# Kernel tuning notes

Hardware: AMD Instinct MI355X
Metric: run time of the kernel (lower is better)

Reference implementation:

```python
import jax, jax.numpy as jnp
import numpy as np

B, T, D, H = 2, 2048, 1024, 16
HS = D // H  # head_size = 64
EPS = 1e-5


def layer_norm(x, g, b):
    mu = jnp.mean(x, axis=-1, keepdims=True)
    var = jnp.var(x, axis=-1, keepdims=True)
    return (x - mu) * jax.lax.rsqrt(var + EPS) * g + b


def setup_inputs() -> dict:
    key = jax.random.key(0)
    ks = jax.random.split(key, 12)
    s_attn = 1.0 / np.sqrt(D)
    s_ff1 = 1.0 / np.sqrt(D)
    s_ff2 = 1.0 / np.sqrt(4 * D)
    return {
        "x": jax.random.normal(ks[0], (B, T, D), jnp.float32),
        "Wq": jax.random.normal(ks[1], (H, D, HS), jnp.float32) * s_attn,
        "Wk": jax.random.normal(ks[2], (H, D, HS), jnp.float32) * s_attn,
        "Wv": jax.random.normal(ks[3], (H, D, HS), jnp.float32) * s_attn,
        "Wo": jax.random.normal(ks[4], (H * HS, D), jnp.float32) * (1.0 / np.sqrt(H * HS)),
        "bo": jnp.zeros((D,), jnp.float32),
        "W1": jax.random.normal(ks[5], (D, 4 * D), jnp.float32) * s_ff1,
        "b1": jnp.zeros((4 * D,), jnp.float32),
        "W2": jax.random.normal(ks[6], (4 * D, D), jnp.float32) * s_ff2,
        "b2": jnp.zeros((D,), jnp.float32),
        "ln1_g": jnp.ones((D,), jnp.float32),
        "ln1_b": jnp.zeros((D,), jnp.float32),
        "ln2_g": jnp.ones((D,), jnp.float32),
        "ln2_b": jnp.zeros((D,), jnp.float32),
    }


def reference(x, Wq, Wk, Wv, Wo, bo, W1, b1, W2, b2, ln1_g, ln1_b, ln2_g, ln2_b):
    # --- self-attention on ln1(x) ---
    h = layer_norm(x, ln1_g, ln1_b)
    Q = jnp.einsum('bsd,hdk->bhsk', h, Wq)
    K = jnp.einsum('bsd,hdk->bhsk', h, Wk)
    V = jnp.einsum('bsd,hdk->bhsk', h, Wv)
    scores = jnp.einsum('bhqk,bhsk->bhqs', Q, K) * (HS ** -0.5)
    attn = jax.nn.softmax(scores, axis=-1)  # [B,H,T,T] non-causal, as in source
    out = jnp.einsum('bhqs,bhsk->bhqk', attn, V)
    out = out.transpose(0, 2, 1, 3).reshape(B, T, H * HS)  # concat heads
    sa = out @ Wo + bo
    x = x + sa
    # --- feed-forward on ln2(x) ---
    h2 = layer_norm(x, ln2_g, ln2_b)
    ff = jax.nn.relu(h2 @ W1 + b1) @ W2 + b2
    return x + ff
```

## Files before the change

kernel.cpp:

```cpp
#include <hip/hip_runtime.h>
#include <cstdint>
#include <cmath>

typedef __bf16 bf16;
typedef __bf16 bf16x8 __attribute__((ext_vector_type(8)));
typedef __bf16 bf16x4 __attribute__((ext_vector_type(4)));
typedef __bf16 bf16x2 __attribute__((ext_vector_type(2)));
typedef float  f32x4  __attribute__((ext_vector_type(4)));

#define B_   2
#define T_   2048
#define D_   1024
#define H_   16
#define HS_  64
#define NTOK (B_ * T_)

typedef __attribute__((address_space(1))) uint8_t* gp1_t;
typedef __attribute__((address_space(3))) uint8_t* lp3_t;
__device__ __forceinline__ void gl_lds16(const void* g, void* l) {
    __builtin_amdgcn_global_load_lds((gp1_t)(uintptr_t)g,
                                     (lp3_t)(uint32_t)(uintptr_t)l,
                                     16, 0, 0);
}

__device__ __forceinline__ f32x4 mfma16(bf16x8 a, bf16x8 b, f32x4 c) {
    return __builtin_amdgcn_mfma_f32_16x16x32_bf16(a, b, c, 0, 0, 0);
}

__device__ __forceinline__ uint32_t pk2(float lo, float hi) {
    bf16x2 t; t[0] = (bf16)lo; t[1] = (bf16)hi;
    return __builtin_bit_cast(uint32_t, t);
}
__device__ __forceinline__ void pl32(uint32_t& a, uint32_t& b) {
    asm("v_permlane32_swap_b32 %0, %1" : "+v"(a), "+v"(b));
}
__device__ __forceinline__ void pl16(uint32_t& a, uint32_t& b) {
    asm("v_permlane16_swap_b32 %0, %1" : "+v"(a), "+v"(b));
}

__global__ void tcast(const float* __restrict__ in, bf16* __restrict__ out,
                      int R, int C) {
    __shared__ float t[32][33];
    const int c0 = blockIdx.x * 32, r0 = blockIdx.y * 32;
    for (int i = 0; i < 4; i++) {
        int r = threadIdx.y + i * 8;
        t[r][threadIdx.x] = in[(size_t)(r0 + r) * C + c0 + threadIdx.x];
    }
    __syncthreads();
    for (int i = 0; i < 4; i++) {
        int rr = threadIdx.y + i * 8;
        out[(size_t)(c0 + rr) * R + r0 + threadIdx.x] = (bf16)t[threadIdx.x][rr];
    }
}

__global__ void qkv_pack(const float* __restrict__ Wq, const float* __restrict__ Wk,
                         const float* __restrict__ Wv, bf16* __restrict__ out) {
    const int z = blockIdx.z;
    const int qkv = z >> 4;
    const float* in = (qkv == 0 ? Wq : qkv == 1 ? Wk : Wv) + (size_t)(z & 15) * D_ * HS_;
    bf16* o = out + (size_t)z * HS_ * D_;
    __shared__ float t[32][33];
    const int c0 = blockIdx.x * 32, r0 = blockIdx.y * 32;
    for (int i = 0; i < 4; i++) {
        int r = threadIdx.y + i * 8;
        t[r][threadIdx.x] = in[(size_t)(r0 + r) * HS_ + c0 + threadIdx.x];
    }
    __syncthreads();
    for (int i = 0; i < 4; i++) {
        int rr = threadIdx.y + i * 8;
        o[(size_t)(c0 + rr) * D_ + r0 + threadIdx.x] = (bf16)t[threadIdx.x][rr];
    }
}

__global__ __launch_bounds__(256) void ln_kernel(const float* __restrict__ x,
                                                 const float* __restrict__ g,
                                                 const float* __restrict__ b,
                                                 bf16* __restrict__ out) {
    const int row = blockIdx.x;
    const int tid = threadIdx.x;
    const float4 v = ((const float4*)(x + (size_t)row * 1024))[tid];
    float s  = v.x + v.y + v.z + v.w;
    float s2 = v.x * v.x + v.y * v.y + v.z * v.z + v.w * v.w;
    for (int m = 1; m < 64; m <<= 1) {
        s  += __shfl_xor(s, m);
        s2 += __shfl_xor(s2, m);
    }
    __shared__ float rs[4], rq[4];
    const int lane = tid & 63, wv = tid >> 6;
    if (lane == 0) { rs[wv] = s; rq[wv] = s2; }
    __syncthreads();
    s  = rs[0] + rs[1] + rs[2] + rs[3];
    s2 = rq[0] + rq[1] + rq[2] + rq[3];
    const float mu   = s * (1.f / 1024.f);
    const float var  = s2 * (1.f / 1024.f) - mu * mu;
    const float rstd = rsqrtf(var + 1e-5f);
    const float4 gg = ((const float4*)g)[tid];
    const float4 bb = ((const float4*)b)[tid];
    bf16x4 o;
    o[0] = (bf16)((v.x - mu) * rstd * gg.x + bb.x);
    o[1] = (bf16)((v.y - mu) * rstd * gg.y + bb.y);
    o[2] = (bf16)((v.z - mu) * rstd * gg.z + bb.z);
    o[3] = (bf16)((v.w - mu) * rstd * gg.w + bb.w);
    *(bf16x4*)(out + (size_t)row * 1024 + tid * 4) = o;
}

__global__ __launch_bounds__(256) void combine4(const float* __restrict__ p0,
                                                const float* __restrict__ p1,
                                                const float* __restrict__ p2,
                                                const float* __restrict__ p3,
                                                const float* __restrict__ resid,
                                                const float* __restrict__ bias,
                                                float* __restrict__ out) {
    const int i4 = blockIdx.x * 256 + threadIdx.x;
    const float4 a = ((const float4*)p0)[i4];
    const float4 b = ((const float4*)p1)[i4];
    const float4 c = ((const float4*)p2)[i4];
    const float4 d = ((const float4*)p3)[i4];
    const float4 r = ((const float4*)resid)[i4];
    const float4 bb = ((const float4*)bias)[i4 & 255];
    float4 o;
    o.x = a.x + b.x + c.x + d.x + r.x + bb.x;
    o.y = a.y + b.y + c.y + d.y + r.y + bb.y;
    o.z = a.z + b.z + c.z + d.z + r.z + bb.z;
    o.w = a.w + b.w + c.w + d.w + r.w + bb.w;
    ((float4*)out)[i4] = o;
}

template <int BIAS, int RELU, int RES, int OUTBF16>
__global__ __launch_bounds__(256, 2) void gemm_bt(
    const bf16* __restrict__ A, const bf16* __restrict__ Bt,
    const float* __restrict__ bias, const float* __restrict__ resid,
    void* __restrict__ Cout, int M, int N, int K) {
    __shared__ __align__(16) bf16 As[2][128 * 32];
    __shared__ __align__(16) bf16 Bs[2][128 * 32];
    const int tid  = threadIdx.x;
    const int lane = tid & 63, w = tid >> 6;
    const int quad = lane >> 4, l15 = lane & 15;
    const int m0 = blockIdx.y * 128, n0 = blockIdx.x * 128;
    const int wm = (w & 1) * 64, wn = (w >> 1) * 64;

    f32x4 acc[4][4];
    for (int i = 0; i < 4; i++)
        for (int j = 0; j < 4; j++) acc[i][j] = f32x4{0.f, 0.f, 0.f, 0.f};

    const int arow = lane >> 2;
    const int acol = (lane & 3) * 8;
    const int c0 = w * 2, c1 = w * 2 + 1;

    for (int kt = 0; kt < K; kt += 64) {
        gl_lds16(A  + (size_t)(m0 + c0 * 16 + arow) * K + kt + acol,      &As[0][c0 * 512]);
        gl_lds16(A  + (size_t)(m0 + c1 * 16 + arow) * K + kt + acol,      &As[0][c1 * 512]);
        gl_lds16(A  + (size_t)(m0 + c0 * 16 + arow) * K + kt + 32 + acol, &As[1][c0 * 512]);
        gl_lds16(A  + (size_t)(m0 + c1 * 16 + arow) * K + kt + 32 + acol, &As[1][c1 * 512]);
        gl_lds16(Bt + (size_t)(n0 + c0 * 16 + arow) * K + kt + acol,      &Bs[0][c0 * 512]);
        gl_lds16(Bt + (size_t)(n0 + c1 * 16 + arow) * K + kt + acol,      &Bs[0][c1 * 512]);
        gl_lds16(Bt + (size_t)(n0 + c0 * 16 + arow) * K + kt + 32 + acol, &Bs[1][c0 * 512]);
        gl_lds16(Bt + (size_t)(n0 + c1 * 16 + arow) * K + kt + 32 + acol, &Bs[1][c1 * 512]);
        __syncthreads();
        for (int kh = 0; kh < 2; kh++) {
            bf16x8 af[4], bfr[4];
            for (int mi = 0; mi < 4; mi++)
                af[mi] = *(const bf16x8*)&As[kh][(wm + mi * 16 + l15) * 32 + quad * 8];
            for (int ni = 0; ni < 4; ni++)
                bfr[ni] = *(const bf16x8*)&Bs[kh][(wn + ni * 16 + l15) * 32 + quad * 8];
            for (int mi = 0; mi < 4; mi++)
                for (int ni = 0; ni < 4; ni++)
                    acc[mi][ni] = mfma16(af[mi], bfr[ni], acc[mi][ni]);
        }
        __syncthreads();
    }

    for (int mi = 0; mi < 4; mi++) {
        for (int ni = 0; ni < 4; ni++) {
            const int colb = n0 + wn + ni * 16 + l15;
            const float bv = BIAS ? bias[colb] : 0.f;
            for (int r = 0; r < 4; r++) {
                const int row = m0 + wm + mi * 16 + quad * 4 + r;
                float v = acc[mi][ni][r] + bv;
                if (RELU) v = fmaxf(v, 0.f);
                if (RES)  v += resid[(size_t)row * N + colb];
                if (OUTBF16) ((bf16*)Cout)[(size_t)row * N + colb] = (bf16)v;
                else         ((float*)Cout)[(size_t)row * N + colb] = v;
            }
        }
    }
}

template <int BIAS, int RELU, int VTP, int PARTIAL>
__global__ __launch_bounds__(512, 2) void gemm256(
    const bf16* __restrict__ A, const bf16* __restrict__ Bt,
    const float* __restrict__ bias, void* __restrict__ Cout,
    bf16* __restrict__ Vt, float* __restrict__ P0, float* __restrict__ P1,
    int M, int N, int K) {
    __shared__ __align__(16) bf16 Asub[4][256 * 32];
    __shared__ __align__(16) bf16 Bsub[4][256 * 32];
    const int tid  = threadIdx.x;
    const int lane = tid & 63, w = tid >> 6;
    const int wr = w >> 2, wc = w & 3;
    const int quad = lane >> 4, l15 = lane & 15;
    const int m0 = blockIdx.y * 256, n0 = blockIdx.x * 256;
    const int kpb = PARTIAL ? (K / (int)gridDim.z) : K;
    const int k0  = PARTIAL ? (int)blockIdx.z * kpb : 0;
    const int S   = kpb / 32;

    const int slog = (((lane & 3) ^ ((lane >> 3) & 3)) * 8);
    const int crow = lane >> 2;
    const bf16* gA0 = A  + (size_t)(m0 + 32 * w + crow)      * K + k0 + slog;
    const bf16* gA1 = A  + (size_t)(m0 + 32 * w + 16 + crow) * K + k0 + slog;
    const bf16* gB0 = Bt + (size_t)(n0 + 32 * w + crow)      * K + k0 + slog;
    const bf16* gB1 = Bt + (size_t)(n0 + 32 * w + 16 + crow) * K + k0 + slog;

    for (int t = 0; t < 3; t++) {
        gl_lds16(gA0, &Asub[t][(32 * w) * 32]);
        gl_lds16(gA1, &Asub[t][(32 * w + 16) * 32]);
        gl_lds16(gB0, &Bsub[t][(32 * w) * 32]);
        gl_lds16(gB1, &Bsub[t][(32 * w + 16) * 32]);
        gA0 += 32; gA1 += 32; gB0 += 32; gB1 += 32;
    }

    f32x4 acc[8][4];
#pragma unroll
    for (int i = 0; i < 8; i++)
#pragma unroll
        for (int j = 0; j < 4; j++) acc[i][j] = f32x4{0.f, 0.f, 0.f, 0.f};

    const int swz = (quad ^ ((l15 >> 1) & 3)) * 8;
    const int aof = (wr * 128 + l15) * 32 + swz;
    const int bof = (wc * 64 + l15) * 32 + swz;

    asm volatile("s_waitcnt vmcnt(8)" ::: "memory");
    __builtin_amdgcn_sched_barrier(0);
    __builtin_amdgcn_s_barrier();

    for (int s = 0; s < S; s++) {
        const bf16* Ab = &Asub[s & 3][0];
        const bf16* Bb = &Bsub[s & 3][0];
        const int pb = (s + 3) & 3;
        bf16x8 af[4], bfr[4];
#pragma unroll
        for (int f = 0; f < 4; f++) af[f] = *(const bf16x8*)&Ab[aof + f * 512];
#pragma unroll
        for (int n = 0; n < 4; n++) bfr[n] = *(const bf16x8*)&Bb[bof + n * 512];
        if (s + 3 < S) {
            gl_lds16(gA0, &Asub[pb][(32 * w) * 32]);
            gl_lds16(gA1, &Asub[pb][(32 * w + 16) * 32]);
            gA0 += 32; gA1 += 32;
        }
        __builtin_amdgcn_sched_barrier(0);
        __builtin_amdgcn_s_barrier();
        asm volatile("s_waitcnt lgkmcnt(0)" ::: "memory");
        __builtin_amdgcn_sched_barrier(0);
        __builtin_amdgcn_s_setprio(1);
#pragma unroll
        for (int f = 0; f < 4; f++)
#pragma unroll
            for (int n = 0; n < 4; n++)
                acc[f][n] = mfma16(af[f], bfr[n], acc[f][n]);
        __builtin_amdgcn_s_setprio(0);
        __builtin_amdgcn_sched_barrier(0);
        __builtin_amdgcn_s_barrier();
#pragma unroll
        for (int f = 0; f < 4; f++) af[f] = *(const bf16x8*)&Ab[aof + 2048 + f * 512];
        if (s + 3 < S) {
            gl_lds16(gB0, &Bsub[pb][(32 * w) * 32]);
            gl_lds16(gB1, &Bsub[pb][(32 * w + 16) * 32]);
            gB0 += 32; gB1 += 32;
        }
        __builtin_amdgcn_sched_barrier(0);
        __builtin_amdgcn_s_barrier();
        asm volatile("s_waitcnt lgkmcnt(0)" ::: "memory");
        __builtin_amdgcn_sched_barrier(0);
        __builtin_amdgcn_s_setprio(1);
#pragma unroll
        for (int f = 0; f < 4; f++)
#pragma unroll
            for (int n = 0; n < 4; n++)
                acc[4 + f][n] = mfma16(af[f], bfr[n], acc[4 + f][n]);
        __builtin_amdgcn_s_setprio(0);
        __builtin_amdgcn_sched_barrier(0);
        if (s <= S - 4)      asm volatile("s_waitcnt vmcnt(8)" ::: "memory");
        else if (s == S - 3) asm volatile("s_waitcnt vmcnt(4)" ::: "memory");
        else if (s == S - 2) asm volatile("s_waitcnt vmcnt(0)" ::: "memory");
        __builtin_amdgcn_s_barrier();
    }

#pragma unroll
    for (int mi = 0; mi < 8; mi++) {
#pragma unroll
        for (int ni = 0; ni < 4; ni++) {
            const int colb = n0 + wc * 64 + ni * 16 + l15;
            const int row0 = m0 + wr * 128 + (mi >> 2) * 64 + (mi & 3) * 16 + quad * 4;
            if (VTP && colb >= 2048) {
                const int h = (colb - 2048) >> 6, hs = (colb - 2048) & 63;
                const int b = row0 >> 11;
                bf16x4 p4;
                p4[0] = (bf16)acc[mi][ni][0];
                p4[1] = (bf16)acc[mi][ni][1];
                p4[2] = (bf16)acc[mi][ni][2];
                p4[3] = (bf16)acc[mi][ni][3];
                *(bf16x4*)&Vt[((size_t)(b * 16 + h) * 64 + hs) * T_ + (row0 & 2047)] = p4;
                continue;
            }
            if (PARTIAL) {
                float* Cz = ((int)blockIdx.z < 2 ? P0 : P1) + (size_t)(blockIdx.z & 1) * M * N;
                for (int r = 0; r < 4; r++)
                    Cz[(size_t)(row0 + r) * N + colb] = acc[mi][ni][r];
            } else {
                const float bv = BIAS ? bias[colb] : 0.f;
                for (int r = 0; r < 4; r++) {
                    float v = acc[mi][ni][r] + bv;
                    if (RELU) v = fmaxf(v, 0.f);
                    ((bf16*)Cout)[(size_t)(row0 + r) * N + colb] = (bf16)v;
                }
            }
        }
    }
}

#define LSTR 68
#define NJ   (T_ / 64)
__global__ __launch_bounds__(256, 2) void flash_attn(const bf16* __restrict__ QKV,
                                                     const bf16* __restrict__ Vt,
                                                     bf16* __restrict__ attn_out) {
    const int bh = blockIdx.y, b = bh >> 4, h = bh & 15;
    const int q0 = blockIdx.x * 128;
    const int tid = threadIdx.x, lane = tid & 63, w = tid >> 6;
    const int quad = lane >> 4, l15 = lane & 15;
    __shared__ __align__(16) bf16 Ks[2][64 * LSTR];
    __shared__ __align__(16) bf16 Vs[2][64 * LSTR];
    const bf16* Qb = QKV + (size_t)b * T_ * 3072 + h * 64;
    const bf16* Kb = QKV + (size_t)b * T_ * 3072 + 1024 + h * 64;
    const bf16* Vb = Vt  + (size_t)bh * HS_ * T_;

    const float sc = 0.125f * 1.44269504088896f;
    const int sr = tid >> 2, scc = (tid & 3) * 16;

    bf16x8 QA[2][2];
    for (int qnt = 0; qnt < 2; qnt++) {
        const size_t row = (size_t)(q0 + w * 32 + qnt * 16 + l15) * 3072;
        for (int kk = 0; kk < 2; kk++) {
            bf16x8 q = *(const bf16x8*)&Qb[row + kk * 32 + quad * 8];
            for (int i = 0; i < 8; i++) q[i] = (bf16)((float)q[i] * sc);
            QA[qnt][kk] = q;
        }
    }

    bf16x8 ones8;
    for (int i = 0; i < 8; i++) ones8[i] = (bf16)1.0f;

    f32x4 O[2][4], lacc[2];
    for (int mi = 0; mi < 2; mi++) {
        lacc[mi] = f32x4{0.f, 0.f, 0.f, 0.f};
        for (int n = 0; n < 4; n++) O[mi][n] = f32x4{0.f, 0.f, 0.f, 0.f};
    }

    *(bf16x8*)&Ks[0][sr * LSTR + scc]     = *(const bf16x8*)&Kb[(size_t)sr * 3072 + scc];
    *(bf16x8*)&Ks[0][sr * LSTR + scc + 8] = *(const bf16x8*)&Kb[(size_t)sr * 3072 + scc + 8];
    *(bf16x8*)&Vs[0][sr * LSTR + scc]     = *(const bf16x8*)&Vb[(size_t)sr * T_ + scc];
    *(bf16x8*)&Vs[0][sr * LSTR + scc + 8] = *(const bf16x8*)&Vb[(size_t)sr * T_ + scc + 8];
    __syncthreads();

    bf16x8 k0, k1, v0, v1;
    for (int j = 0; j < NJ; j++) {
        const int buf = j & 1;
        if (j + 1 < NJ) {
            const int s1 = (j + 1) * 64;
            k0 = *(const bf16x8*)&Kb[(size_t)(s1 + sr) * 3072 + scc];
            k1 = *(const bf16x8*)&Kb[(size_t)(s1 + sr) * 3072 + scc + 8];
            v0 = *(const bf16x8*)&Vb[(size_t)sr * T_ + s1 + scc];
            v1 = *(const bf16x8*)&Vb[(size_t)sr * T_ + s1 + scc + 8];
        }
        bf16x8 KB[4][2];
#pragma unroll
        for (int smt = 0; smt < 4; smt++)
#pragma unroll
            for (int kk = 0; kk < 2; kk++)
                KB[smt][kk] = *(const bf16x8*)&Ks[buf][(smt * 16 + l15) * LSTR + kk * 32 + quad * 8];

        bf16x8 PA[2][2];
#pragma unroll
        for (int qnt = 0; qnt < 2; qnt++) {
            f32x4 ST[4];
#pragma unroll
            for (int smt = 0; smt < 4; smt++) ST[smt] = f32x4{0.f, 0.f, 0.f, 0.f};
            __builtin_amdgcn_s_setprio(1);
#pragma unroll
            for (int kk = 0; kk < 2; kk++)
#pragma unroll
                for (int smt = 0; smt < 4; smt++)
                    ST[smt] = mfma16(KB[smt][kk], QA[qnt][kk], ST[smt]);
            __builtin_amdgcn_s_setprio(0);
            uint32_t w00 = pk2(__builtin_amdgcn_exp2f(ST[0][0]), __builtin_amdgcn_exp2f(ST[0][1]));
            uint32_t w01 = pk2(__builtin_amdgcn_exp2f(ST[0][2]), __builtin_amdgcn_exp2f(ST[0][3]));
            uint32_t w10 = pk2(__builtin_amdgcn_exp2f(ST[1][0]), __builtin_amdgcn_exp2f(ST[1][1]));
            uint32_t w11 = pk2(__builtin_amdgcn_exp2f(ST[1][2]), __builtin_amdgcn_exp2f(ST[1][3]));
            uint32_t w20 = pk2(__builtin_amdgcn_exp2f(ST[2][0]), __builtin_amdgcn_exp2f(ST[2][1]));
            uint32_t w21 = pk2(__builtin_amdgcn_exp2f(ST[2][2]), __builtin_amdgcn_exp2f(ST[2][3]));
            uint32_t w30 = pk2(__builtin_amdgcn_exp2f(ST[3][0]), __builtin_amdgcn_exp2f(ST[3][1]));
            uint32_t w31 = pk2(__builtin_amdgcn_exp2f(ST[3][2]), __builtin_amdgcn_exp2f(ST[3][3]));
            pl32(w00, w10); pl16(w00, w10);
            pl32(w01, w11); pl16(w01, w11);
            pl32(w20, w30); pl16(w20, w30);
            pl32(w21, w31); pl16(w21, w31);
            union { uint32_t u[4]; bf16x8 v; } pa0, pa1;
            pa0.u[0] = w00; pa0.u[1] = w01; pa0.u[2] = w10; pa0.u[3] = w11;
            pa1.u[0] = w20; pa1.u[1] = w21; pa1.u[2] = w30; pa1.u[3] = w31;
            PA[qnt][0] = pa0.v;
            PA[qnt][1] = pa1.v;
        }
        bf16x8 VB[4][2];
#pragma unroll
        for (int n = 0; n < 4; n++)
#pragma unroll
            for (int kk = 0; kk < 2; kk++)
                VB[n][kk] = *(const bf16x8*)&Vs[buf][(n * 16 + l15) * LSTR + kk * 32 + quad * 8];
        __builtin_amdgcn_s_setprio(1);
#pragma unroll
        for (int mi = 0; mi < 2; mi++) {
            const bf16x8 PA0 = PA[mi][0];
            const bf16x8 PA1 = PA[mi][1];
#pragma unroll
            for (int n = 0; n < 4; n++) {
                O[mi][n] = mfma16(PA0, VB[n][0], O[mi][n]);
                O[mi][n] = mfma16(PA1, VB[n][1], O[mi][n]);
            }
            lacc[mi] = mfma16(PA0, ones8, lacc[mi]);
            lacc[mi] = mfma16(PA1, ones8, lacc[mi]);
        }
        __builtin_amdgcn_s_setprio(0);
        if (j + 1 < NJ) {
            *(bf16x8*)&Ks[buf ^ 1][sr * LSTR + scc]     = k0;
            *(bf16x8*)&Ks[buf ^ 1][sr * LSTR + scc + 8] = k1;
            *(bf16x8*)&Vs[buf ^ 1][sr * LSTR + scc]     = v0;
            *(bf16x8*)&Vs[buf ^ 1][sr * LSTR + scc + 8] = v1;
        }
        __syncthreads();
    }

    for (int mi = 0; mi < 2; mi++) {
        for (int r = 0; r < 4; r++) {
            const float inv = 1.f / lacc[mi][r];
            const size_t tok = (size_t)b * T_ + q0 + w * 32 + mi * 16 + quad * 4 + r;
            for (int n = 0; n < 4; n++)
                attn_out[tok * 1024 + h * 64 + n * 16 + l15] = (bf16)(O[mi][n][r] * inv);
        }
    }
}

extern "C" void kernel_launch(void* const* d_in, const int* in_sizes, int n_in,
                              void* d_out, int out_size, void* d_ws, size_t ws_size,
                              hipStream_t stream) {
    const float* x   = (const float*)d_in[0];
    const float* Wq  = (const float*)d_in[1];
    const float* Wk  = (const float*)d_in[2];
    const float* Wv  = (const float*)d_in[3];
    const float* Wo  = (const float*)d_in[4];
    const float* bo  = (const float*)d_in[5];
    const float* W1  = (const float*)d_in[6];
    const float* b1  = (const float*)d_in[7];
    const float* W2  = (const float*)d_in[8];
    const float* b2  = (const float*)d_in[9];
    const float* g1  = (const float*)d_in[10];
    const float* be1 = (const float*)d_in[11];
    const float* g2  = (const float*)d_in[12];
    const float* be2 = (const float*)d_in[13];

    char* ws = (char*)d_ws;
    const size_t MB = 1ull << 20;
    bf16*  WqkvT = (bf16*)(ws);
    bf16*  WoT   = (bf16*)(ws + 6  * MB);
    bf16*  W1T   = (bf16*)(ws + 8  * MB);
    bf16*  W2T   = (bf16*)(ws + 16 * MB);
    bf16*  hbuf  = (bf16*)(ws + 24 * MB);
    bf16*  QKV   = (bf16*)(ws + 32 * MB);
    bf16*  Vt    = (bf16*)(ws + 56 * MB);
    bf16*  attn  = (bf16*)(ws + 64 * MB);
    float* x2    = (float*)(ws + 72 * MB);
    bf16*  ff1   = (bf16*)(ws + 32 * MB);
    float* partA = (float*)(ws);
    float* partB = (float*)(ws + 88 * MB);
    float* out   = (float*)d_out;

    dim3 tb(32, 8);
    qkv_pack<<<dim3(2, 32, 48), tb, 0, stream>>>(Wq, Wk, Wv, WqkvT);
    tcast<<<dim3(32, 32),  tb, 0, stream>>>(Wo, WoT, 1024, 1024);
    tcast<<<dim3(128, 32), tb, 0, stream>>>(W1, W1T, 1024, 4096);
    tcast<<<dim3(32, 128), tb, 0, stream>>>(W2, W2T, 4096, 1024);
    ln_kernel<<<NTOK, 256, 0, stream>>>(x, g1, be1, hbuf);
    gemm256<0, 0, 1, 0><<<dim3(12, 16), 512, 0, stream>>>(
        hbuf, WqkvT, nullptr, QKV, Vt, nullptr, nullptr, NTOK, 3072, 1024);
    flash_attn<<<dim3(T_ / 128, B_ * H_), 256, 0, stream>>>(QKV, Vt, attn);
    gemm_bt<1, 0, 1, 0><<<dim3(8, 32), 256, 0, stream>>>(attn, WoT, bo, x, x2, NTOK, 1024, 1024);
    ln_kernel<<<NTOK, 256, 0, stream>>>(x2, g2, be2, hbuf);
    gemm256<1, 1, 0, 0><<<dim3(16, 16), 512, 0, stream>>>(
        hbuf, W1T, b1, ff1, nullptr, nullptr, nullptr, NTOK, 4096, 1024);
    gemm256<0, 0, 0, 1><<<dim3(4, 16, 4), 512, 0, stream>>>(
        ff1, W2T, nullptr, nullptr, nullptr, partA, partB, NTOK, 1024, 4096);
    combine4<<<NTOK, 256, 0, stream>>>(partA, partA + (size_t)NTOK * 1024,
                                       partB, partB + (size_t)NTOK * 1024,
                                       x2, b2, out);
}
```

Measured before the change: 341.1 us.

## Fuse weight prep and LN1 into one launch; use 128-tile GEMM for QKV

Merges the four weight transpose/cast kernels and the first layernorm into a single launch, with branches selected by block index. This removes several launch gaps. The QKV projection moves from the 256-tile gemm256 kernel (192 blocks) to the 128-tile gemm_bt kernel (768 blocks), which gains a V-transpose epilogue so the machine's CUs are better filled. The trade-off is a smaller tile with less data reuse per block, and a divergent, heterogeneous prep kernel.

```diff
diff --git a/kernel.cpp b/kernel.cpp
--- a/kernel.cpp
+++ b/kernel.cpp
@@ -38,37 +38,79 @@
     asm("v_permlane16_swap_b32 %0, %1" : "+v"(a), "+v"(b));
 }
 
-__global__ void tcast(const float* __restrict__ in, bf16* __restrict__ out,
-                      int R, int C) {
+__global__ __launch_bounds__(256) void prep_fused(
+    const float* __restrict__ Wq, const float* __restrict__ Wk,
+    const float* __restrict__ Wv, const float* __restrict__ Wo,
+    const float* __restrict__ W1, const float* __restrict__ W2,
+    const float* __restrict__ x,  const float* __restrict__ g,
+    const float* __restrict__ be,
+    bf16* __restrict__ WqkvT, bf16* __restrict__ WoT,
+    bf16* __restrict__ W1T,  bf16* __restrict__ W2T,
+    bf16* __restrict__ hbuf) {
+    const int bid = blockIdx.x;
+    const int tid = threadIdx.x;
+
+    if (bid >= 12288) {
+        const int row = bid - 12288;
+        const float4 v = ((const float4*)(x + (size_t)row * 1024))[tid];
+        float s  = v.x + v.y + v.z + v.w;
+        float s2 = v.x * v.x + v.y * v.y + v.z * v.z + v.w * v.w;
+        for (int m = 1; m < 64; m <<= 1) {
+            s  += __shfl_xor(s, m);
+            s2 += __shfl_xor(s2, m);
+        }
+        __shared__ float rs[4], rq[4];
+        const int lane = tid & 63, wv = tid >> 6;
+        if (lane == 0) { rs[wv] = s; rq[wv] = s2; }
+        __syncthreads();
+        s  = rs[0] + rs[1] + rs[2] + rs[3];
+        s2 = rq[0] + rq[1] + rq[2] + rq[3];
+        const float mu   = s * (1.f / 1024.f);
+        const float var  = s2 * (1.f / 1024.f) - mu * mu;
+        const float rstd = rsqrtf(var + 1e-5f);
+        const float4 gg = ((const float4*)g)[tid];
+        const float4 bb = ((const float4*)be)[tid];
+        bf16x4 o;
+        o[0] = (bf16)((v.x - mu) * rstd * gg.x + bb.x);
+        o[1] = (bf16)((v.y - mu) * rstd * gg.y + bb.y);
+        o[2] = (bf16)((v.z - mu) * rstd * gg.z + bb.z);
+        o[3] = (bf16)((v.w - mu) * rstd * gg.w + bb.w);
+        *(bf16x4*)(hbuf + (size_t)row * 1024 + tid * 4) = o;
+        return;
+    }
+
+    const float* in; bf16* out;
+    int C, R, bx, by;
+    if (bid < 3072) {
+        const int z = bid >> 6, rem = bid & 63;
+        bx = rem & 1; by = rem >> 1;
+        C = HS_; R = D_;
+        in  = (z < 16 ? Wq : z < 32 ? Wk : Wv) + (size_t)(z & 15) * D_ * HS_;
+        out = WqkvT + (size_t)z * HS_ * D_;
+    } else if (bid < 4096) {
+        const int rem = bid - 3072;
+        bx = rem & 31; by = rem >> 5;
+        C = 1024; R = 1024; in = Wo; out = WoT;
+    } else if (bid < 8192) {
+        const int rem = bid - 4096;
+        bx = rem & 127; by = rem >> 7;
+        C = 4096; R = 1024; in = W1; out = W1T;
+    } else {
+        const int rem = bid - 8192;
+        bx = rem & 31; by = rem >> 5;
+        C = 1024; R = 4096; in = W2; out = W2T;
+    }
+    const int tx = tid & 31, ty = tid >> 5;
+    const int c0 = bx * 32, r0 = by * 32;
     __shared__ float t[32][33];
-    const int c0 = blockIdx.x * 32, r0 = blockIdx.y * 32;
     for (int i = 0; i < 4; i++) {
-        int r = threadIdx.y + i * 8;
-        t[r][threadIdx.x] = in[(size_t)(r0 + r) * C + c0 + threadIdx.x];
+        int r = ty + i * 8;
+        t[r][tx] = in[(size_t)(r0 + r) * C + c0 + tx];
     }
     __syncthreads();
     for (int i = 0; i < 4; i++) {
-        int rr = threadIdx.y + i * 8;
-        out[(size_t)(c0 + rr) * R + r0 + threadIdx.x] = (bf16)t[threadIdx.x][rr];
-    }
-}
-
-__global__ void qkv_pack(const float* __restrict__ Wq, const float* __restrict__ Wk,
-                         const float* __restrict__ Wv, bf16* __restrict__ out) {
-    const int z = blockIdx.z;
-    const int qkv = z >> 4;
-    const float* in = (qkv == 0 ? Wq : qkv == 1 ? Wk : Wv) + (size_t)(z & 15) * D_ * HS_;
-    bf16* o = out + (size_t)z * HS_ * D_;
-    __shared__ float t[32][33];
-    const int c0 = blockIdx.x * 32, r0 = blockIdx.y * 32;
-    for (int i = 0; i < 4; i++) {
-        int r = threadIdx.y + i * 8;
-        t[r][threadIdx.x] = in[(size_t)(r0 + r) * HS_ + c0 + threadIdx.x];
-    }
-    __syncthreads();
-    for (int i = 0; i < 4; i++) {
-        int rr = threadIdx.y + i * 8;
-        o[(size_t)(c0 + rr) * D_ + r0 + threadIdx.x] = (bf16)t[threadIdx.x][rr];
+        int rr = ty + i * 8;
+        out[(size_t)(c0 + rr) * R + r0 + tx] = (bf16)t[tx][rr];
     }
 }
 
@@ -126,11 +168,11 @@
     ((float4*)out)[i4] = o;
 }
 
-template <int BIAS, int RELU, int RES, int OUTBF16>
+template <int BIAS, int RELU, int RES, int OUTBF16, int VTP = 0>
 __global__ __launch_bounds__(256, 2) void gemm_bt(
     const bf16* __restrict__ A, const bf16* __restrict__ Bt,
     const float* __restrict__ bias, const float* __restrict__ resid,
-    void* __restrict__ Cout, int M, int N, int K) {
+    void* __restrict__ Cout, bf16* __restrict__ Vt, int M, int N, int K) {
     __shared__ __align__(16) bf16 As[2][128 * 32];
     __shared__ __align__(16) bf16 Bs[2][128 * 32];
     const int tid  = threadIdx.x;
@@ -173,6 +215,18 @@
     for (int mi = 0; mi < 4; mi++) {
         for (int ni = 0; ni < 4; ni++) {
             const int colb = n0 + wn + ni * 16 + l15;
+            if (VTP && colb >= 2048) {
+                const int h = (colb - 2048) >> 6, hs = (colb - 2048) & 63;
+                const int row0 = m0 + wm + mi * 16 + quad * 4;
+                const int b = row0 >> 11;
+                bf16x4 p4;
+                p4[0] = (bf16)acc[mi][ni][0];
+                p4[1] = (bf16)acc[mi][ni][1];
+                p4[2] = (bf16)acc[mi][ni][2];
+                p4[3] = (bf16)acc[mi][ni][3];
+                *(bf16x4*)&Vt[((size_t)(b * 16 + h) * 64 + hs) * T_ + (row0 & 2047)] = p4;
+                continue;
+            }
             const float bv = BIAS ? bias[colb] : 0.f;
             for (int r = 0; r < 4; r++) {
                 const int row = m0 + wm + mi * 16 + quad * 4 + r;
@@ -481,16 +535,13 @@
     float* partB = (float*)(ws + 88 * MB);
     float* out   = (float*)d_out;
 
-    dim3 tb(32, 8);
-    qkv_pack<<<dim3(2, 32, 48), tb, 0, stream>>>(Wq, Wk, Wv, WqkvT);
-    tcast<<<dim3(32, 32),  tb, 0, stream>>>(Wo, WoT, 1024, 1024);
-    tcast<<<dim3(128, 32), tb, 0, stream>>>(W1, W1T, 1024, 4096);
-    tcast<<<dim3(32, 128), tb, 0, stream>>>(W2, W2T, 4096, 1024);
-    ln_kernel<<<NTOK, 256, 0, stream>>>(x, g1, be1, hbuf);
-    gemm256<0, 0, 1, 0><<<dim3(12, 16), 512, 0, stream>>>(
-        hbuf, WqkvT, nullptr, QKV, Vt, nullptr, nullptr, NTOK, 3072, 1024);
+    prep_fused<<<16384, 256, 0, stream>>>(Wq, Wk, Wv, Wo, W1, W2, x, g1, be1,
+                                          WqkvT, WoT, W1T, W2T, hbuf);
+    gemm_bt<0, 0, 0, 1, 1><<<dim3(24, 32), 256, 0, stream>>>(
+        hbuf, WqkvT, nullptr, nullptr, QKV, Vt, NTOK, 3072, 1024);
     flash_attn<<<dim3(T_ / 128, B_ * H_), 256, 0, stream>>>(QKV, Vt, attn);
-    gemm_bt<1, 0, 1, 0><<<dim3(8, 32), 256, 0, stream>>>(attn, WoT, bo, x, x2, NTOK, 1024, 1024);
+    gemm_bt<1, 0, 1, 0><<<dim3(8, 32), 256, 0, stream>>>(
+        attn, WoT, bo, x, x2, nullptr, NTOK, 1024, 1024);
     ln_kernel<<<NTOK, 256, 0, stream>>>(x2, g2, be2, hbuf);
     gemm256<1, 1, 0, 0><<<dim3(16, 16), 512, 0, stream>>>(
         hbuf, W1T, b1, ff1, nullptr, nullptr, nullptr, NTOK, 4096, 1024);
```

After: 339.1 us. No clear change (-0.6%).
